# Performance work log

Hardware: AMD Instinct MI355X
Metric: run time of the kernel (lower is better)

The kernel has to match this reference:

```python
import jax, jax.numpy as jnp
import numpy as np

# ---- module constants (from init_kwargs) ----
VOXEL_SIZE = np.array([0.1, 0.1, 0.2], np.float32)
PC_RANGE = np.array([0.0, -40.0, -3.0, 70.4, 40.0, 1.0], np.float32)
MAX_PTS = 10            # max_points_in_voxel
MAX_VOX = 40000         # max_voxel_num (hard voxelization cap per sample)
GRID = np.round((PC_RANGE[3:] - PC_RANGE[:3]) / VOXEL_SIZE).astype(np.int32)  # [704,800,20] (x,y,z)
BIG = int(GRID[0]) * int(GRID[1]) * int(GRID[2])

PC_MIN = jnp.asarray(PC_RANGE[:3])
VSIZE = jnp.asarray(VOXEL_SIZE)
GRID_J = jnp.asarray(GRID)

B = 8
N_PER_B = 120000


def setup_inputs() -> dict:
    key = jax.random.key(0)
    k1, = jax.random.split(key, 1)
    u = jax.random.uniform(k1, (B * N_PER_B, 4), dtype=jnp.float32)
    # place points inside (and slightly around) pc_range
    x = u[:, 0] * 72.0 - 0.5
    y = u[:, 1] * 82.0 - 41.0
    z = u[:, 2] * 4.4 - 3.2
    inten = u[:, 3]
    bs_idx = jnp.repeat(jnp.arange(B, dtype=jnp.float32), N_PER_B)
    points = jnp.stack([bs_idx, x, y, z, inten], axis=1)  # [960000, 5]
    return {"points": points, "batch_size": B}


def _voxelize_one(pts):
    """Hard voxelization of one point cloud pts [N,4] -> fixed-size buffers.
    Faithful to first-come voxel ordering and per-voxel point caps."""
    N = pts.shape[0]
    idxs = jnp.arange(N, dtype=jnp.int32)
    xyz = pts[:, :3]
    c = jnp.floor((xyz - PC_MIN) / VSIZE).astype(jnp.int32)  # [N,3] (x,y,z)
    valid = jnp.all((c >= 0) & (c < GRID_J), axis=1)
    lid = (c[:, 2] * GRID[1] + c[:, 1]) * GRID[0] + c[:, 0]  # z-major linear id
    lid = jnp.where(valid, lid, BIG)

    order = jnp.argsort(lid)            # stable: within a voxel, original order kept
    lid_s = lid[order]
    is_new = jnp.concatenate([jnp.ones((1,), bool), lid_s[1:] != lid_s[:-1]])
    gid = jnp.cumsum(is_new.astype(jnp.int32)) - 1           # group id per sorted point
    starts = jax.lax.cummax(jnp.where(is_new, idxs, 0))      # group start position
    pos = idxs - starts                                      # rank inside its voxel

    g_lid = jax.ops.segment_min(lid_s, gid, num_segments=N)
    g_valid = g_lid < BIG
    first_orig = jax.ops.segment_min(order.astype(jnp.int32), gid, num_segments=N)
    # voxel slot = first-appearance rank (invalid/empty groups pushed to the end)
    first_key = jnp.where(g_valid, first_orig, N + idxs)
    perm = jnp.argsort(first_key)
    slot = jnp.zeros(N, jnp.int32).at[perm].set(idxs)

    pslot = slot[gid]
    keep = g_valid[gid] & (pslot < MAX_VOX) & (pos < MAX_PTS)
    sslot = jnp.where(keep, pslot, MAX_VOX)   # overflow bucket, sliced off
    spos = jnp.where(keep, pos, 0)
    voxels = jnp.zeros((MAX_VOX + 1, MAX_PTS, pts.shape[1]), pts.dtype)
    voxels = voxels.at[sslot, spos].set(pts[order])[:MAX_VOX]

    gcount = jax.ops.segment_sum(keep.astype(jnp.int32), gid, num_segments=N)
    gslot = jnp.where(g_valid & (slot < MAX_VOX), slot, MAX_VOX)
    num_points = jnp.zeros(MAX_VOX + 1, jnp.int32).at[gslot].set(gcount)[:MAX_VOX]

    cs = c[order]
    gz = jax.ops.segment_min(cs[:, 2], gid, num_segments=N)
    gy = jax.ops.segment_min(cs[:, 1], gid, num_segments=N)
    gx = jax.ops.segment_min(cs[:, 0], gid, num_segments=N)
    coors = jnp.full((MAX_VOX + 1, 3), -1, jnp.int32)
    coors = coors.at[gslot].set(jnp.stack([gz, gy, gx], axis=1))[:MAX_VOX]  # (z,y,x)
    return voxels, num_points, coors


def reference(points, batch_size):
    feats = points[:, 1:]
    n_per_b = feats.shape[0] // batch_size  # points constructed contiguously per sample
    pts = feats.reshape(batch_size, n_per_b, feats.shape[1])
    voxels_b, num_b, coors_b = jax.vmap(_voxelize_one)(pts)
    voxels = voxels_b.reshape(batch_size * MAX_VOX, MAX_PTS, feats.shape[1])
    num_points = num_b.reshape(-1)
    batch_col = jnp.repeat(jnp.arange(batch_size, dtype=jnp.int32), MAX_VOX)[:, None]
    coors_batch = jnp.concatenate([batch_col, coors_b.reshape(-1, 3)], axis=1)  # [b,z,y,x]
    grid_size = jnp.asarray(GRID)
    return voxels, num_points, coors_batch, grid_size
```

## Files before the change

### kernel.cpp

```cpp
#include <hip/hip_runtime.h>

#define NB        8
#define NPB       120000
#define NPTS      (NB * NPB)
#define MAX_PTS   10
#define MAX_VOX   40000
#define GX        704
#define GY        800
#define GZ        20
#define CELLS     (GX * GY * GZ)
#define WPB       (CELLS / 32)

#define HC2       (1 << 15)
#define HMASK2    (HC2 - 1)
#define NSLOT2    (NB * HC2)
#define TILES     469
#define TILES_PAD 512
#define MBCAP     8192
#define MTILE     2048

#define EMPTY64   0xFFFFFFFFFFFFFFFFull

#define OUT_VOX   0LL
#define OUT_NUM   12800000LL
#define OUT_COOR  13120000LL
#define OUT_GRID  14400000LL

__device__ __forceinline__ bool point_cell(const float* __restrict__ p,
                                           int& cx, int& cy, int& cz) {
    cx = (int)floorf((p[1] - 0.0f)   / 0.1f);
    cy = (int)floorf((p[2] - (-40.0f)) / 0.1f);
    cz = (int)floorf((p[3] - (-3.0f))  / 0.2f);
    return (cx >= 0) & (cx < GX) & (cy >= 0) & (cy < GY) & (cz >= 0) & (cz < GZ);
}

__global__ void k_init(float* __restrict__ out, uint4* __restrict__ bm4,
                       ulonglong2* __restrict__ slab2, unsigned* __restrict__ mcount) {
    int t = blockIdx.x * blockDim.x + threadIdx.x;
    int stride = gridDim.x * blockDim.x;
    uint4 z4 = make_uint4(0u, 0u, 0u, 0u);
    for (int i = t; i < NB * WPB / 4; i += stride) bm4[i] = z4;
    ulonglong2 e2; e2.x = EMPTY64; e2.y = EMPTY64;
    for (int i = t; i < NSLOT2 / 2; i += stride) slab2[i] = e2;
    if (t < NB) mcount[t * 16] = 0u;
    if (t == 0) {
        out[OUT_GRID + 0] = 704.f;
        out[OUT_GRID + 1] = 800.f;
        out[OUT_GRID + 2] = 20.f;
    }
}

__global__ void k_phase1(const float* __restrict__ pts, unsigned* __restrict__ bm,
                         unsigned long long* __restrict__ slabB,
                         unsigned char* __restrict__ flag) {
    int g = blockIdx.x * blockDim.x + threadIdx.x;
    if (g >= NPTS) return;
    int b = g / NPB;
    int idx = g - b * NPB;
    const float* p = pts + (long long)g * 5;
    int cx, cy, cz;
    if (!point_cell(p, cx, cy, cz)) { flag[g] = 0; return; }
    int lid = (cz * GY + cy) * GX + cx;
    unsigned mask = 1u << (lid & 31);
    unsigned old = atomicOr(&bm[b * WPB + (lid >> 5)], mask);
    if ((old & mask) == 0u) {
        flag[g] = 1;
    } else {
        flag[g] = 0;
        unsigned h = (((unsigned)lid * 2654435761u) >> 17) & HMASK2;
        unsigned long long key = ((unsigned long long)(unsigned)lid << 32)
                               | (unsigned long long)(unsigned)idx;
        int base2 = b * HC2;
        while (true) {
            unsigned long long* wp = &slabB[base2 + (int)h];
            unsigned long long cur = *((volatile unsigned long long*)wp);
            if (cur == EMPTY64) {
                unsigned long long o = atomicCAS(wp, EMPTY64, key);
                if (o == EMPTY64) break;
                cur = o;
            }
            if ((unsigned)(cur >> 32) == (unsigned)lid) { atomicMin(wp, key); break; }
            h = (h + 1) & HMASK2;
        }
    }
}

__global__ void k_phase2(const float* __restrict__ pts, unsigned char* __restrict__ flag,
                         unsigned long long* __restrict__ slabB) {
    int g = blockIdx.x * blockDim.x + threadIdx.x;
    if (g >= NPTS) return;
    if (!flag[g]) return;
    int b = g / NPB;
    int idx = g - b * NPB;
    const float* p = pts + (long long)g * 5;
    int cx, cy, cz;
    point_cell(p, cx, cy, cz);
    int lid = (cz * GY + cy) * GX + cx;
    unsigned h = (((unsigned)lid * 2654435761u) >> 17) & HMASK2;
    int base2 = b * HC2;
    while (true) {
        unsigned long long cur = slabB[base2 + (int)h];
        if (cur == EMPTY64) break;
        if ((unsigned)(cur >> 32) == (unsigned)lid) {
            unsigned long long key = ((unsigned long long)(unsigned)lid << 32)
                                   | (unsigned long long)(unsigned)idx;
            unsigned long long old = atomicMin(&slabB[base2 + (int)h], key);
            unsigned omin = (unsigned)old;
            if (omin < (unsigned)idx) {
                flag[g] = 0;
                flag[b * NPB + (int)omin] = 2;
            } else {
                flag[g] = 2;
            }
            break;
        }
        h = (h + 1) & HMASK2;
    }
}

__global__ void k_leader_scan(const unsigned char* __restrict__ flag,
                              unsigned char* __restrict__ rank8, int* __restrict__ tileSum) {
    int b = blockIdx.y;
    int tile = blockIdx.x;
    int idx = tile * 256 + threadIdx.x;
    int f = 0;
    if (idx < NPB) f = flag[b * NPB + idx] ? 1 : 0;
    __shared__ int sc[256];
    sc[threadIdx.x] = f;
    __syncthreads();
    for (int off = 1; off < 256; off <<= 1) {
        int v = sc[threadIdx.x];
        if ((int)threadIdx.x >= off) v += sc[threadIdx.x - off];
        __syncthreads();
        sc[threadIdx.x] = v;
        __syncthreads();
    }
    if (idx < NPB) rank8[b * NPB + idx] = (unsigned char)(sc[threadIdx.x] - f);
    if (threadIdx.x == 255) tileSum[b * TILES_PAD + tile] = sc[255];
}

__global__ void k_scan_tiles(const int* __restrict__ tileSum, int* __restrict__ tileOff) {
    int b = blockIdx.x;
    int t = threadIdx.x;
    __shared__ int sc[512];
    int v = (t < TILES) ? tileSum[b * TILES_PAD + t] : 0;
    sc[t] = v;
    __syncthreads();
    for (int off = 1; off < 512; off <<= 1) {
        int x = sc[t];
        if (t >= off) x += sc[t - off];
        __syncthreads();
        sc[t] = x;
        __syncthreads();
    }
    if (t < TILES) tileOff[b * TILES_PAD + t] = sc[t] - v;
}

__global__ void k_finish(const float* __restrict__ pts, const unsigned char* __restrict__ flag,
                         const unsigned char* __restrict__ rank8, const int* __restrict__ tileOff,
                         const unsigned long long* __restrict__ slabB,
                         float* __restrict__ out, int2* __restrict__ mlist,
                         unsigned* __restrict__ mcount) {
    int g = blockIdx.x * blockDim.x + threadIdx.x;
    if (g >= NPTS) return;
    int b = g / NPB;
    int idx = g - b * NPB;
    const float* p = pts + (long long)g * 5;
    int cx, cy, cz;
    if (!point_cell(p, cx, cy, cz)) return;
    unsigned char fl = flag[g];
    if (fl) {
        int slot = tileOff[b * TILES_PAD + (idx >> 8)] + (int)rank8[g];
        if (slot >= MAX_VOX) return;
        long long r = (long long)b * MAX_VOX + slot;
        ((float4*)(out + OUT_COOR))[r] = make_float4((float)b, (float)cz, (float)cy, (float)cx);
        out[OUT_NUM + r] = 1.f;
        float4* row = (float4*)(out + OUT_VOX + r * (MAX_PTS * 4));
        row[0] = make_float4(p[1], p[2], p[3], p[4]);
        float4 zf = make_float4(0.f, 0.f, 0.f, 0.f);
        #pragma unroll
        for (int i = 1; i < MAX_PTS; i++) row[i] = zf;
    } else {
        int lid = (cz * GY + cy) * GX + cx;
        unsigned h = (((unsigned)lid * 2654435761u) >> 17) & HMASK2;
        int base2 = b * HC2;
        unsigned minidx;
        while (true) {
            unsigned long long cur = slabB[base2 + (int)h];
            if ((unsigned)(cur >> 32) == (unsigned)lid) { minidx = (unsigned)cur; break; }
            h = (h + 1) & HMASK2;
        }
        int slot = tileOff[b * TILES_PAD + ((int)minidx >> 8)] + (int)rank8[b * NPB + (int)minidx];
        if (slot >= MAX_VOX) return;
        unsigned m = atomicAdd(&mcount[b * 16], 1u);
        if (m < MBCAP) mlist[(size_t)b * MBCAP + m] = make_int2(slot, idx);
    }
}

__global__ void k_multi(const float* __restrict__ pts,
                        const int2* __restrict__ mlist, const unsigned* __restrict__ mcount,
                        float* __restrict__ out) {
    int b = blockIdx.y;
    unsigned n = mcount[b * 16];
    if (n > MBCAP) n = MBCAP;
    unsigned t = blockIdx.x * blockDim.x + threadIdx.x;
    const int2* lst = mlist + (size_t)b * MBCAP;
    bool active = (t < n);
    int2 e = active ? lst[t] : make_int2(-1, -1);
    int pos = 1;
    int same = 0;
    __shared__ int2 sm[MTILE];
    for (unsigned chunk = 0; chunk < n; chunk += MTILE) {
        unsigned m = n - chunk;
        if (m > MTILE) m = MTILE;
        for (unsigned i = threadIdx.x; i < m; i += 256)
            sm[i] = lst[chunk + i];
        __syncthreads();
        if (active) {
            #pragma unroll 4
            for (unsigned j = 0; j < m; j++) {
                int2 o = sm[j];
                if (o.x == e.x) { same++; if (o.y < e.y) pos++; }
            }
        }
        __syncthreads();
    }
    if (!active) return;
    if (pos == 1) {
        int cnt = same + 1;
        out[OUT_NUM + (long long)b * MAX_VOX + e.x] =
            (float)(cnt < MAX_PTS ? cnt : MAX_PTS);
    }
    if (pos >= MAX_PTS) return;
    const float* p = pts + ((long long)b * NPB + e.y) * 5;
    ((float4*)(out + OUT_VOX))[(long long)(b * MAX_VOX + e.x) * MAX_PTS + pos] =
        make_float4(p[1], p[2], p[3], p[4]);
}

extern "C" void kernel_launch(void* const* d_in, const int* in_sizes, int n_in,
                              void* d_out, int out_size, void* d_ws, size_t ws_size,
                              hipStream_t stream) {
    const float* pts = (const float*)d_in[0];
    float* out = (float*)d_out;

    char* w = (char*)d_ws;
    unsigned* bm = (unsigned*)w;              w += (size_t)NB * WPB * 4;
    unsigned long long* slabB = (unsigned long long*)w;
    w += (size_t)NSLOT2 * 8;
    unsigned char* flag = (unsigned char*)w;  w += (size_t)NPTS;
    unsigned char* rank8 = (unsigned char*)w; w += (size_t)NPTS;
    int* tileSum = (int*)w;  w += (size_t)NB * TILES_PAD * 4;
    int* tileOff = (int*)w;  w += (size_t)NB * TILES_PAD * 4;
    int2* mlist = (int2*)w;  w += (size_t)NB * MBCAP * 8;
    unsigned* mcount = (unsigned*)w; w += (size_t)NB * 16 * 4;

    k_init<<<dim3(2048), dim3(256), 0, stream>>>(out, (uint4*)bm, (ulonglong2*)slabB, mcount);
    k_phase1<<<dim3((NPTS + 255) / 256), dim3(256), 0, stream>>>(pts, bm, slabB, flag);
    k_phase2<<<dim3((NPTS + 255) / 256), dim3(256), 0, stream>>>(pts, flag, slabB);
    k_leader_scan<<<dim3(TILES, NB), dim3(256), 0, stream>>>(flag, rank8, tileSum);
    k_scan_tiles<<<dim3(NB), dim3(512), 0, stream>>>(tileSum, tileOff);
    k_finish<<<dim3((NPTS + 255) / 256), dim3(256), 0, stream>>>(pts, flag, rank8, tileOff,
                                                                 slabB, out, mlist, mcount);
    k_multi<<<dim3(MBCAP / 256, NB), dim3(256), 0, stream>>>(pts, mlist, mcount, out);
}
```

Baseline: 163.1 us.

## Fuse tile-offset scan into leader scan via last-block pattern; interleave batches across blocks

Removes the separate k_scan_tiles launch. The last block to finish each batch's leader scan, detected with an atomic done counter and a threadfence, now scans the tile sums and writes the tile offsets. Phase kernels also map block indices so consecutive blocks cycle through batches. This spreads atomic and hash-table traffic across the per-batch structures and removes the b=g/NPB division. It costs an extra atomic per block and 2KB more shared memory in the scan kernel.

```diff
diff --git a/kernel.cpp b/kernel.cpp
--- a/kernel.cpp
+++ b/kernel.cpp
@@ -35,14 +35,15 @@
 }
 
 __global__ void k_init(float* __restrict__ out, uint4* __restrict__ bm4,
-                       ulonglong2* __restrict__ slab2, unsigned* __restrict__ mcount) {
+                       ulonglong2* __restrict__ slab2, unsigned* __restrict__ mcount,
+                       unsigned* __restrict__ done) {
     int t = blockIdx.x * blockDim.x + threadIdx.x;
     int stride = gridDim.x * blockDim.x;
     uint4 z4 = make_uint4(0u, 0u, 0u, 0u);
     for (int i = t; i < NB * WPB / 4; i += stride) bm4[i] = z4;
     ulonglong2 e2; e2.x = EMPTY64; e2.y = EMPTY64;
     for (int i = t; i < NSLOT2 / 2; i += stride) slab2[i] = e2;
-    if (t < NB) mcount[t * 16] = 0u;
+    if (t < NB) { mcount[t * 16] = 0u; done[t * 16] = 0u; }
     if (t == 0) {
         out[OUT_GRID + 0] = 704.f;
         out[OUT_GRID + 1] = 800.f;
@@ -53,10 +54,10 @@
 __global__ void k_phase1(const float* __restrict__ pts, unsigned* __restrict__ bm,
                          unsigned long long* __restrict__ slabB,
                          unsigned char* __restrict__ flag) {
-    int g = blockIdx.x * blockDim.x + threadIdx.x;
-    if (g >= NPTS) return;
-    int b = g / NPB;
-    int idx = g - b * NPB;
+    int b = blockIdx.x & 7;
+    int idx = (blockIdx.x >> 3) * 256 + threadIdx.x;
+    if (idx >= NPB) return;
+    int g = b * NPB + idx;
     const float* p = pts + (long long)g * 5;
     int cx, cy, cz;
     if (!point_cell(p, cx, cy, cz)) { flag[g] = 0; return; }
@@ -87,11 +88,11 @@
 
 __global__ void k_phase2(const float* __restrict__ pts, unsigned char* __restrict__ flag,
                          unsigned long long* __restrict__ slabB) {
-    int g = blockIdx.x * blockDim.x + threadIdx.x;
-    if (g >= NPTS) return;
+    int b = blockIdx.x & 7;
+    int idx = (blockIdx.x >> 3) * 256 + threadIdx.x;
+    if (idx >= NPB) return;
+    int g = b * NPB + idx;
     if (!flag[g]) return;
-    int b = g / NPB;
-    int idx = g - b * NPB;
     const float* p = pts + (long long)g * 5;
     int cx, cy, cz;
     point_cell(p, cx, cy, cz);
@@ -119,13 +120,16 @@
 }
 
 __global__ void k_leader_scan(const unsigned char* __restrict__ flag,
-                              unsigned char* __restrict__ rank8, int* __restrict__ tileSum) {
+                              unsigned char* __restrict__ rank8, int* __restrict__ tileSum,
+                              int* __restrict__ tileOff, unsigned* __restrict__ done) {
     int b = blockIdx.y;
     int tile = blockIdx.x;
     int idx = tile * 256 + threadIdx.x;
     int f = 0;
     if (idx < NPB) f = flag[b * NPB + idx] ? 1 : 0;
     __shared__ int sc[256];
+    __shared__ int s2[512];
+    __shared__ int sLast;
     sc[threadIdx.x] = f;
     __syncthreads();
     for (int off = 1; off < 256; off <<= 1) {
@@ -136,24 +140,29 @@
         __syncthreads();
     }
     if (idx < NPB) rank8[b * NPB + idx] = (unsigned char)(sc[threadIdx.x] - f);
-    if (threadIdx.x == 255) tileSum[b * TILES_PAD + tile] = sc[255];
-}
-
-__global__ void k_scan_tiles(const int* __restrict__ tileSum, int* __restrict__ tileOff) {
-    int b = blockIdx.x;
-    int t = threadIdx.x;
-    __shared__ int sc[512];
-    int v = (t < TILES) ? tileSum[b * TILES_PAD + t] : 0;
-    sc[t] = v;
+    if (threadIdx.x == 255) {
+        tileSum[b * TILES_PAD + tile] = sc[255];
+        __threadfence();
+        unsigned d = atomicAdd(&done[b * 16], 1u);
+        sLast = (d == (unsigned)(TILES - 1)) ? 1 : 0;
+    }
+    __syncthreads();
+    if (!sLast) return;
+    volatile const int* ts = tileSum + b * TILES_PAD;
+    int t0 = threadIdx.x, t1 = threadIdx.x + 256;
+    int o0 = (t0 < TILES) ? ts[t0] : 0;
+    int o1 = (t1 < TILES) ? ts[t1] : 0;
+    s2[t0] = o0; s2[t1] = o1;
     __syncthreads();
     for (int off = 1; off < 512; off <<= 1) {
-        int x = sc[t];
-        if (t >= off) x += sc[t - off];
-        __syncthreads();
-        sc[t] = x;
-        __syncthreads();
-    }
-    if (t < TILES) tileOff[b * TILES_PAD + t] = sc[t] - v;
+        int v0 = s2[t0] + ((t0 >= off) ? s2[t0 - off] : 0);
+        int v1 = s2[t1] + ((t1 >= off) ? s2[t1 - off] : 0);
+        __syncthreads();
+        s2[t0] = v0; s2[t1] = v1;
+        __syncthreads();
+    }
+    if (t0 < TILES) tileOff[b * TILES_PAD + t0] = s2[t0] - o0;
+    if (t1 < TILES) tileOff[b * TILES_PAD + t1] = s2[t1] - o1;
 }
 
 __global__ void k_finish(const float* __restrict__ pts, const unsigned char* __restrict__ flag,
@@ -161,10 +170,10 @@
                          const unsigned long long* __restrict__ slabB,
                          float* __restrict__ out, int2* __restrict__ mlist,
                          unsigned* __restrict__ mcount) {
-    int g = blockIdx.x * blockDim.x + threadIdx.x;
-    if (g >= NPTS) return;
-    int b = g / NPB;
-    int idx = g - b * NPB;
+    int b = blockIdx.x & 7;
+    int idx = (blockIdx.x >> 3) * 256 + threadIdx.x;
+    if (idx >= NPB) return;
+    int g = b * NPB + idx;
     const float* p = pts + (long long)g * 5;
     int cx, cy, cz;
     if (!point_cell(p, cx, cy, cz)) return;
@@ -253,13 +262,13 @@
     int* tileOff = (int*)w;  w += (size_t)NB * TILES_PAD * 4;
     int2* mlist = (int2*)w;  w += (size_t)NB * MBCAP * 8;
     unsigned* mcount = (unsigned*)w; w += (size_t)NB * 16 * 4;
-
-    k_init<<<dim3(2048), dim3(256), 0, stream>>>(out, (uint4*)bm, (ulonglong2*)slabB, mcount);
-    k_phase1<<<dim3((NPTS + 255) / 256), dim3(256), 0, stream>>>(pts, bm, slabB, flag);
-    k_phase2<<<dim3((NPTS + 255) / 256), dim3(256), 0, stream>>>(pts, flag, slabB);
-    k_leader_scan<<<dim3(TILES, NB), dim3(256), 0, stream>>>(flag, rank8, tileSum);
-    k_scan_tiles<<<dim3(NB), dim3(512), 0, stream>>>(tileSum, tileOff);
-    k_finish<<<dim3((NPTS + 255) / 256), dim3(256), 0, stream>>>(pts, flag, rank8, tileOff,
-                                                                 slabB, out, mlist, mcount);
+    unsigned* done = (unsigned*)w;   w += (size_t)NB * 16 * 4;
+
+    const int PB = TILES * NB;
+    k_init<<<dim3(2048), dim3(256), 0, stream>>>(out, (uint4*)bm, (ulonglong2*)slabB, mcount, done);
+    k_phase1<<<dim3(PB), dim3(256), 0, stream>>>(pts, bm, slabB, flag);
+    k_phase2<<<dim3(PB), dim3(256), 0, stream>>>(pts, flag, slabB);
+    k_leader_scan<<<dim3(TILES, NB), dim3(256), 0, stream>>>(flag, rank8, tileSum, tileOff, done);
+    k_finish<<<dim3(PB), dim3(256), 0, stream>>>(pts, flag, rank8, tileOff, slabB, out, mlist, mcount);
     k_multi<<<dim3(MBCAP / 256, NB), dim3(256), 0, stream>>>(pts, mlist, mcount, out);
 }
```

Result: slower. 223.1 us (+36.8%).
